# Optimization experiments

Hardware: AMD Instinct MI355X
Metric: run time of the kernel (lower is better)

The kernel has to match this reference:

```python
import jax, jax.numpy as jnp
import numpy as np

B, N, D, M, H = 16, 2048, 512, 512, 8
DH = D // H
PDE_STEPS = 3
DT = 0.01


def layer_norm(x, g, b, eps=1e-5):
    mu = x.mean(-1, keepdims=True)
    v = ((x - mu) ** 2).mean(-1, keepdims=True)
    return (x - mu) * jax.lax.rsqrt(v + eps) * g + b


def laplacian1d(f):
    # f: [B, M, D]; Neumann boundary via edge padding
    fp = jnp.pad(f, ((0, 0), (1, 1), (0, 0)), mode='edge')
    return fp[:, :-2] - 2.0 * fp[:, 1:-1] + fp[:, 2:]


def diffuse(f, coef, steps=PDE_STEPS, dt=DT):
    # explicit-Euler diffusion PDE evolution, per-channel coefficient
    for _ in range(steps):
        f = f + dt * coef * laplacian1d(f)
    return f


def setup_inputs() -> dict:
    key = jax.random.key(0)
    ks = jax.random.split(key, 10)
    s = 0.02
    return {
        'embeddings': jax.random.normal(ks[0], (B, N, D), dtype=jnp.float32),
        'positions': jax.random.uniform(ks[1], (B, N, 1), dtype=jnp.float32),
        'sigma': jnp.asarray(0.1, dtype=jnp.float32),
        'alpha': s * jax.random.normal(ks[2], (H, H), dtype=jnp.float32),
        'w_int': s * jax.random.normal(ks[3], (D, D), dtype=jnp.float32),
        'b_int': jnp.zeros((D,), dtype=jnp.float32),
        'diff_coef': 0.5 * jnp.ones((D,), dtype=jnp.float32),
        'W1': s * jax.random.normal(ks[4], (D, D), dtype=jnp.float32),
        'b1': jnp.zeros((D,), dtype=jnp.float32),
        'W2': s * jax.random.normal(ks[5], (D, D), dtype=jnp.float32),
        'b2': jnp.zeros((D,), dtype=jnp.float32),
        'evo_coef': 0.5 * jnp.ones((D,), dtype=jnp.float32),
        'ln1_g': jnp.ones((D,), dtype=jnp.float32),
        'ln1_b': jnp.zeros((D,), dtype=jnp.float32),
        'Wout': s * jax.random.normal(ks[6], (D, D), dtype=jnp.float32),
        'bout': jnp.zeros((D,), dtype=jnp.float32),
        'ln2_g': jnp.ones((D,), dtype=jnp.float32),
        'ln2_b': jnp.zeros((D,), dtype=jnp.float32),
    }


def reference(embeddings, positions, sigma, alpha, w_int, b_int, diff_coef,
              W1, b1, W2, b2, evo_coef, ln1_g, ln1_b, Wout, bout, ln2_g, ln2_b):
    # 1) RBF field projection onto uniform 1D grid in [0,1]
    grid = jnp.linspace(0.0, 1.0, M, dtype=embeddings.dtype)  # [M]
    d2 = (grid[None, :, None] - positions[..., 0][:, None, :]) ** 2  # [B,M,N]
    K = jnp.exp(-d2 / (2.0 * sigma ** 2))
    field = jnp.einsum('bmn,bnd->bmd', K, embeddings)  # [B,M,D]
    # 2) multi-head field interference: learned cross-head coupling + proj
    Fh = field.reshape(B, M, H, DH)
    mix = jnp.einsum('hk,bmkd->bmhd', alpha, Fh).reshape(B, M, D)
    field = field + mix @ w_int + b_int
    # 3) field propagation: diffusion PDE steps
    field = diffuse(field, diff_coef)
    # 4) interaction operator: pointwise gated MLP with residual
    field = field + jax.nn.gelu(field @ W1 + b1) @ W2 + b2
    # 5) field evolution: further diffusion PDE steps
    field = diffuse(field, evo_coef)
    # 6) linear field sampling back at token positions
    u = jnp.clip(positions[..., 0], 0.0, 1.0) * (M - 1)  # [B,N]
    i0 = jnp.clip(jnp.floor(u), 0, M - 2).astype(jnp.int32)
    w = (u - i0.astype(u.dtype))[..., None]  # [B,N,1]
    f0 = jnp.take_along_axis(field, i0[:, :, None], axis=1)  # [B,N,D]
    f1 = jnp.take_along_axis(field, (i0 + 1)[:, :, None], axis=1)
    sampled = (1.0 - w) * f0 + w * f1
    # 7) residual + LN, output proj (dropout=eval/identity), residual + LN
    enh = layer_norm(sampled + embeddings, ln1_g, ln1_b)
    out = enh @ Wout + bout
    out = layer_norm(out + enh, ln2_g, ln2_b)
    return out
```

## Files before the change

### kernel.cpp

```cpp
#include <hip/hip_runtime.h>
#include <hip/hip_bf16.h>
#include <math.h>

#define BB 16
#define NN 2048
#define DD 512
#define MM 512

typedef __attribute__((ext_vector_type(8))) short bf16x8;
typedef __attribute__((ext_vector_type(4))) float f32x4;

__device__ __forceinline__ short f2b(float x) {
  union { __hip_bfloat16 h; short s; } u; u.h = __float2bfloat16(x); return u.s;
}
__device__ __forceinline__ float b2f(short s) {
  union { short s2; __hip_bfloat16 h; } u; u.s2 = s; return __bfloat162float(u.h);
}
__device__ __forceinline__ float gelu_f(float x) {
  float x3 = x * x * x;
  return 0.5f * x * (1.0f + tanhf(0.79788456080286536f * (x + 0.044715f * x3)));
}

template<int BM, int BN, int NT, int WR, int WC, int ACT, int RES,
         bool BIAS, bool WB32, bool WB16, bool BATCH>
__global__ __launch_bounds__(NT) void gemm_mfma(
    const short* __restrict__ A, const short* __restrict__ BT,
    const float* __restrict__ bias, const void* __restrict__ res,
    float* __restrict__ C, short* __restrict__ Cb, int K)
{
  constexpr int WAVES = NT / 64;
  constexpr int MF = BM / WR / 16;
  constexpr int NF = BN / WC / 16;
  constexpr int WMT = BM / WR;
  constexpr int WNT = BN / WC;
  constexpr int CHA = BM / 16;
  constexpr int CHB = BN / 16;

  __shared__ short As[2][BM * 32];
  __shared__ short Bs[2][BN * 32];

  const int tid = threadIdx.x;
  const int wid = tid >> 6, lane = tid & 63;
  const int lrow = lane & 15, kg = lane >> 4;
  const int wr = (WR == 1) ? 0 : (wid >> 1);
  const int wc = (WR == 1) ? wid : (wid & 1);

  int r0, c0, z;
  if constexpr (BATCH) {
    z = blockIdx.x; r0 = blockIdx.y * BM; c0 = blockIdx.z * BN;
  } else {
    z = 0; r0 = blockIdx.x * BM; c0 = blockIdx.y * BN;
  }
  const size_t zA  = BATCH ? (size_t)z * MM * K : 0;
  const size_t zBT = BATCH ? (size_t)z * DD * K : 0;
  const size_t zC  = BATCH ? (size_t)z * MM * DD : 0;

  auto stage = [&](int bf, int kc) {
    #pragma unroll
    for (int i = 0; i < CHB / WAVES; ++i) {
      const int ch = wid * (CHB / WAVES) + i;
      const int col = ch * 16 + (lane >> 2);
      const short* gp = BT + zBT + (size_t)(c0 + col) * K + kc + (lane & 3) * 8;
      __builtin_amdgcn_global_load_lds(
          (const __attribute__((address_space(1))) void*)gp,
          (__attribute__((address_space(3))) void*)&Bs[bf][ch * 512], 16, 0, 0);
    }
    if constexpr (CHA >= WAVES) {
      #pragma unroll
      for (int i = 0; i < CHA / WAVES; ++i) {
        const int ch = wid * (CHA / WAVES) + i;
        const int row = ch * 16 + (lane >> 2);
        const short* gp = A + zA + (size_t)(r0 + row) * K + kc + (lane & 3) * 8;
        __builtin_amdgcn_global_load_lds(
            (const __attribute__((address_space(1))) void*)gp,
            (__attribute__((address_space(3))) void*)&As[bf][ch * 512], 16, 0, 0);
      }
    } else {
      if (wid < CHA) {
        const int row = wid * 16 + (lane >> 2);
        const short* gp = A + zA + (size_t)(r0 + row) * K + kc + (lane & 3) * 8;
        __builtin_amdgcn_global_load_lds(
            (const __attribute__((address_space(1))) void*)gp,
            (__attribute__((address_space(3))) void*)&As[bf][wid * 512], 16, 0, 0);
      }
    }
  };

  f32x4 acc[MF][NF];
  #pragma unroll
  for (int m = 0; m < MF; ++m)
    #pragma unroll
    for (int n = 0; n < NF; ++n) acc[m][n] = (f32x4){0.f, 0.f, 0.f, 0.f};

  stage(0, 0);
  __syncthreads();

  int buf = 0;
  for (int kc = 0; kc < K; kc += 32) {
    if (kc + 32 < K) stage(buf ^ 1, kc + 32);

    bf16x8 af[MF], bfv[NF];
    #pragma unroll
    for (int m = 0; m < MF; ++m)
      af[m] = *(const bf16x8*)&As[buf][(wr * WMT + m * 16 + lrow) * 32 + kg * 8];
    #pragma unroll
    for (int n = 0; n < NF; ++n)
      bfv[n] = *(const bf16x8*)&Bs[buf][(wc * WNT + n * 16 + lrow) * 32 + kg * 8];
    #pragma unroll
    for (int m = 0; m < MF; ++m)
      #pragma unroll
      for (int n = 0; n < NF; ++n)
        acc[m][n] = __builtin_amdgcn_mfma_f32_16x16x32_bf16(af[m], bfv[n], acc[m][n], 0, 0, 0);

    __syncthreads();
    buf ^= 1;
  }

  #pragma unroll
  for (int m = 0; m < MF; ++m) {
    #pragma unroll
    for (int n = 0; n < NF; ++n) {
      const int col = c0 + wc * WNT + n * 16 + lrow;
      const int row0 = r0 + wr * WMT + m * 16 + kg * 4;
      float bi = 0.0f;
      if constexpr (BIAS) bi = bias[col];
      #pragma unroll
      for (int r = 0; r < 4; ++r) {
        float x = acc[m][n][r] + bi;
        if constexpr (ACT == 1) x = gelu_f(x);
        const size_t off = zC + (size_t)(row0 + r) * DD + col;
        if constexpr (RES == 1) x += ((const float*)res)[off];
        if constexpr (RES == 2) x += b2f(((const short*)res)[off]);
        if constexpr (WB32) C[off] = x;
        if constexpr (WB16) Cb[off] = f2b(x);
      }
    }
  }
}

__global__ __launch_bounds__(512) void gemm_out_ln(
    const short* __restrict__ A, const short* __restrict__ BT,
    const float* __restrict__ bias, const float* __restrict__ g,
    const float* __restrict__ be, float* __restrict__ out)
{
  constexpr int BM = 64, BN = 512, K = 512;
  constexpr int WAVES = 8, CHB = BN / 16, CHA = BM / 16;

  __shared__ short As[2][BM * 32];
  __shared__ short Bs[2][BN * 32];
  __shared__ float redS[8][64], redQ[8][64];
  __shared__ float lnMu[64], lnIs[64];

  const int tid = threadIdx.x;
  const int wid = tid >> 6, lane = tid & 63;
  const int lrow = lane & 15, kg = lane >> 4;
  const int wc = wid;
  const int r0 = blockIdx.x * BM;

  auto stage = [&](int bf, int kc) {
    #pragma unroll
    for (int i = 0; i < CHB / WAVES; ++i) {
      const int ch = wid * (CHB / WAVES) + i;
      const int col = ch * 16 + (lane >> 2);
      const short* gp = BT + (size_t)col * K + kc + (lane & 3) * 8;
      __builtin_amdgcn_global_load_lds(
          (const __attribute__((address_space(1))) void*)gp,
          (__attribute__((address_space(3))) void*)&Bs[bf][ch * 512], 16, 0, 0);
    }
    if (wid < CHA) {
      const int row = wid * 16 + (lane >> 2);
      const short* gp = A + (size_t)(r0 + row) * K + kc + (lane & 3) * 8;
      __builtin_amdgcn_global_load_lds(
          (const __attribute__((address_space(1))) void*)gp,
          (__attribute__((address_space(3))) void*)&As[bf][wid * 512], 16, 0, 0);
    }
  };

  f32x4 acc[4][4];
  #pragma unroll
  for (int m = 0; m < 4; ++m)
    #pragma unroll
    for (int n = 0; n < 4; ++n) acc[m][n] = (f32x4){0.f, 0.f, 0.f, 0.f};

  stage(0, 0);
  __syncthreads();
  int buf = 0;
  for (int kc = 0; kc < K; kc += 32) {
    if (kc + 32 < K) stage(buf ^ 1, kc + 32);
    bf16x8 af[4], bfv[4];
    #pragma unroll
    for (int m = 0; m < 4; ++m)
      af[m] = *(const bf16x8*)&As[buf][(m * 16 + lrow) * 32 + kg * 8];
    #pragma unroll
    for (int n = 0; n < 4; ++n)
      bfv[n] = *(const bf16x8*)&Bs[buf][(wc * 64 + n * 16 + lrow) * 32 + kg * 8];
    #pragma unroll
    for (int m = 0; m < 4; ++m)
      #pragma unroll
      for (int n = 0; n < 4; ++n)
        acc[m][n] = __builtin_amdgcn_mfma_f32_16x16x32_bf16(af[m], bfv[n], acc[m][n], 0, 0, 0);
    __syncthreads();
    buf ^= 1;
  }

  #pragma unroll
  for (int m = 0; m < 4; ++m) {
    #pragma unroll
    for (int n = 0; n < 4; ++n) {
      const float bi = bias[wc * 64 + n * 16 + lrow];
      #pragma unroll
      for (int r = 0; r < 4; ++r) acc[m][n][r] += bi;
    }
  }
  #pragma unroll
  for (int m = 0; m < 4; ++m) {
    #pragma unroll
    for (int r = 0; r < 4; ++r) {
      float ps = acc[m][0][r] + acc[m][1][r] + acc[m][2][r] + acc[m][3][r];
      float pq = acc[m][0][r] * acc[m][0][r] + acc[m][1][r] * acc[m][1][r] +
                 acc[m][2][r] * acc[m][2][r] + acc[m][3][r] * acc[m][3][r];
      #pragma unroll
      for (int off = 8; off >= 1; off >>= 1) {
        ps += __shfl_xor(ps, off);
        pq += __shfl_xor(pq, off);
      }
      if (lrow == 0) {
        redS[wid][m * 16 + kg * 4 + r] = ps;
        redQ[wid][m * 16 + kg * 4 + r] = pq;
      }
    }
  }
  __syncthreads();
  if (tid < 64) {
    float s = 0.f, q = 0.f;
    #pragma unroll
    for (int w = 0; w < 8; ++w) { s += redS[w][tid]; q += redQ[w][tid]; }
    const float mu = s * (1.0f / 512.0f);
    const float var = q * (1.0f / 512.0f) - mu * mu;
    lnMu[tid] = mu;
    lnIs[tid] = rsqrtf(var + 1e-5f);
  }
  __syncthreads();
  #pragma unroll
  for (int m = 0; m < 4; ++m) {
    #pragma unroll
    for (int n = 0; n < 4; ++n) {
      const int col = wc * 64 + n * 16 + lrow;
      const float gc = g[col], bc = be[col];
      #pragma unroll
      for (int r = 0; r < 4; ++r) {
        const int row = m * 16 + kg * 4 + r;
        out[(size_t)(r0 + row) * DD + col] =
            (acc[m][n][r] - lnMu[row]) * lnIs[row] * gc + bc;
      }
    }
  }
}

__global__ __launch_bounds__(256) void kmat_kernel(
    const float* __restrict__ pos, const float* __restrict__ sigp,
    short* __restrict__ Kmat)
{
  const int gid = blockIdx.x * 256 + threadIdx.x;
  const int n8 = gid & 255;
  const int m  = (gid >> 8) & (MM - 1);
  const int b  = gid >> 17;
  const float s = sigp[0];
  const float inv2s2 = 1.0f / (2.0f * s * s);
  const float g = (float)m * (1.0f / 511.0f);
  const float* pp = pos + (size_t)b * NN + n8 * 8;
  const float4 p0 = *(const float4*)pp;
  const float4 p1 = *(const float4*)(pp + 4);
  const float pv[8] = {p0.x, p0.y, p0.z, p0.w, p1.x, p1.y, p1.z, p1.w};
  bf16x8 o;
  #pragma unroll
  for (int j = 0; j < 8; ++j) {
    const float d = g - pv[j];
    o[j] = f2b(__expf(-(d * d) * inv2s2));
  }
  *(bf16x8*)&Kmat[((size_t)b * MM + m) * NN + n8 * 8] = o;
}

__global__ __launch_bounds__(256) void wtrans_kernel(
    const float* __restrict__ w0, const float* __restrict__ w1,
    const float* __restrict__ w2, const float* __restrict__ w3,
    short* __restrict__ outW)
{
  __shared__ float tle[32][33];
  const int z = blockIdx.z;
  const float* W = (z == 0) ? w0 : (z == 1) ? w1 : (z == 2) ? w2 : w3;
  short* WT = outW + (size_t)z * DD * DD;
  const int bx = blockIdx.x * 32;
  const int by = blockIdx.y * 32;
  const int t = threadIdx.x;
  const int r = t >> 3, c4 = (t & 7) * 4;
  const float4 v = *(const float4*)(W + (size_t)(bx + r) * DD + by + c4);
  tle[r][c4 + 0] = v.x; tle[r][c4 + 1] = v.y; tle[r][c4 + 2] = v.z; tle[r][c4 + 3] = v.w;
  __syncthreads();
  short4 o;
  #pragma unroll
  for (int j = 0; j < 4; ++j) {
    float val = tle[c4 + j][r];
    if (z == 3 && (bx + c4 + j) == (by + r)) val += 1.0f;
    ((short*)&o)[j] = f2b(val);
  }
  *(short4*)(WT + (size_t)(by + r) * DD + bx + c4) = o;
}

__global__ __launch_bounds__(256) void embtrans_kernel(
    const float* __restrict__ emb, short* __restrict__ embT)
{
  __shared__ float tle[32][33];
  const int z = blockIdx.z;
  const int bx = blockIdx.x * 32;
  const int by = blockIdx.y * 32;
  const int t = threadIdx.x;
  const int r = t >> 3, c4 = (t & 7) * 4;
  const float4 v = *(const float4*)(emb + ((size_t)z * NN + bx + r) * DD + by + c4);
  tle[r][c4 + 0] = v.x; tle[r][c4 + 1] = v.y; tle[r][c4 + 2] = v.z; tle[r][c4 + 3] = v.w;
  __syncthreads();
  const short4 o = make_short4(f2b(tle[c4 + 0][r]), f2b(tle[c4 + 1][r]),
                               f2b(tle[c4 + 2][r]), f2b(tle[c4 + 3][r]));
  *(short4*)(embT + ((size_t)z * DD + by + r) * NN + bx + c4) = o;
}

__global__ __launch_bounds__(256) void mix_kernel(
    const float* __restrict__ field, const float* __restrict__ alpha,
    short* __restrict__ mixout)
{
  __shared__ float row[DD];
  __shared__ float al[64];
  const size_t r = blockIdx.x;
  const int t = threadIdx.x;
  const float* fr = field + r * DD;
  *(float2*)&row[t * 2] = *(const float2*)&fr[t * 2];
  if (t < 64) al[t] = alpha[t];
  __syncthreads();
  const int j = t * 2;
  const int h = j >> 6;
  const int jj = j & 63;
  float s0 = 0.0f, s1 = 0.0f;
  #pragma unroll
  for (int k = 0; k < 8; ++k) {
    const float a = al[h * 8 + k];
    const float2 v = *(const float2*)&row[k * 64 + jj];
    s0 += a * v.x;
    s1 += a * v.y;
  }
  *(short2*)&mixout[r * DD + j] = make_short2(f2b(s0), f2b(s1));
}

__device__ __forceinline__ float4 dstep(float4 fm, float4 f, float4 fp, float4 a) {
  float4 o;
  o.x = f.x + a.x * (fm.x - 2.0f * f.x + fp.x);
  o.y = f.y + a.y * (fm.y - 2.0f * f.y + fp.y);
  o.z = f.z + a.z * (fm.z - 2.0f * f.z + fp.z);
  o.w = f.w + a.w * (fm.w - 2.0f * f.w + fp.w);
  return o;
}

template<bool WB16>
__global__ __launch_bounds__(256) void diffuse3_kernel(
    const float* __restrict__ in, float* __restrict__ out,
    const float* __restrict__ coef, short* __restrict__ bfout)
{
  const size_t base = ((size_t)blockIdx.x * 256 + threadIdx.x) * 4;
  const int d = (int)(base & (DD - 1));
  const int m = (int)((base >> 9) & (MM - 1));
  const size_t rowbase = base - (size_t)m * DD;

  float4 u[7];
  #pragma unroll
  for (int o = 0; o < 7; ++o) {
    int mm = m + o - 3;
    mm = mm < 0 ? 0 : (mm > MM - 1 ? MM - 1 : mm);
    u[o] = *(const float4*)(in + rowbase + (size_t)mm * DD);
  }
  const float4 c = *(const float4*)(coef + d);
  float4 a;
  a.x = 0.01f * c.x; a.y = 0.01f * c.y; a.z = 0.01f * c.z; a.w = 0.01f * c.w;

  float4 v[5];
  #pragma unroll
  for (int o = 0; o < 5; ++o) v[o] = dstep(u[o], u[o + 1], u[o + 2], a);
  float4 w2[3];
  #pragma unroll
  for (int o = 0; o < 3; ++o) w2[o] = dstep(v[o], v[o + 1], v[o + 2], a);
  const float4 r = dstep(w2[0], w2[1], w2[2], a);

  *(float4*)(out + base) = r;
  if constexpr (WB16) {
    *(short4*)(bfout + base) = make_short4(f2b(r.x), f2b(r.y), f2b(r.z), f2b(r.w));
  }
}

__device__ __forceinline__ void ln_stats_512(float sum, float sq, float& mu, float& inv_std) {
  #pragma unroll
  for (int off = 32; off >= 1; off >>= 1) {
    sum += __shfl_down(sum, off);
    sq  += __shfl_down(sq,  off);
  }
  __shared__ float red[8];
  __shared__ float mv[2];
  const int lane = threadIdx.x & 63;
  const int wid = threadIdx.x >> 6;
  if (lane == 0) { red[wid] = sum; red[4 + wid] = sq; }
  __syncthreads();
  if (threadIdx.x == 0) {
    float ts = red[0] + red[1] + red[2] + red[3];
    float tq = red[4] + red[5] + red[6] + red[7];
    float m = ts * (1.0f / 512.0f);
    float v = tq * (1.0f / 512.0f) - m * m;
    mv[0] = m;
    mv[1] = rsqrtf(v + 1e-5f);
  }
  __syncthreads();
  mu = mv[0];
  inv_std = mv[1];
}

__global__ __launch_bounds__(256) void sample_ln_kernel(
    const float* __restrict__ field, const float* __restrict__ pos,
    const float* __restrict__ emb, const float* __restrict__ g,
    const float* __restrict__ be, short* __restrict__ enhb)
{
  const size_t row = blockIdx.x;
  const int b = (int)(row >> 11);
  const int t = threadIdx.x;

  const float p = pos[row];
  const float u = fminf(fmaxf(p, 0.0f), 1.0f) * 511.0f;
  int i0 = (int)floorf(u);
  if (i0 > MM - 2) i0 = MM - 2;
  if (i0 < 0) i0 = 0;
  const float w = u - (float)i0;

  const float* f0 = field + ((size_t)b * MM + i0) * DD;
  const int j = t * 2;
  const float2 a0 = *(const float2*)(f0 + j);
  const float2 a1 = *(const float2*)(f0 + DD + j);
  const float2 e = *(const float2*)(emb + row * DD + j);
  const float sx = (1.0f - w) * a0.x + w * a1.x + e.x;
  const float sy = (1.0f - w) * a0.y + w * a1.y + e.y;

  float mu, is;
  ln_stats_512(sx + sy, sx * sx + sy * sy, mu, is);

  const float2 gg = *(const float2*)(g + j);
  const float2 bb2 = *(const float2*)(be + j);
  *(short2*)&enhb[row * DD + j] = make_short2(
      f2b((sx - mu) * is * gg.x + bb2.x),
      f2b((sy - mu) * is * gg.y + bb2.y));
}


extern "C" void kernel_launch(void* const* d_in, const int* in_sizes, int n_in,
                              void* d_out, int out_size, void* d_ws, size_t ws_size,
                              hipStream_t stream)
{
  const float* emb   = (const float*)d_in[0];
  const float* pos   = (const float*)d_in[1];
  const float* sigma = (const float*)d_in[2];
  const float* alpha = (const float*)d_in[3];
  const float* w_int = (const float*)d_in[4];
  const float* b_int = (const float*)d_in[5];
  const float* diffc = (const float*)d_in[6];
  const float* W1    = (const float*)d_in[7];
  const float* b1    = (const float*)d_in[8];
  const float* W2    = (const float*)d_in[9];
  const float* b2    = (const float*)d_in[10];
  const float* evoc  = (const float*)d_in[11];
  const float* ln1g  = (const float*)d_in[12];
  const float* ln1b  = (const float*)d_in[13];
  const float* Wout  = (const float*)d_in[14];
  const float* bout  = (const float*)d_in[15];
  const float* ln2g  = (const float*)d_in[16];
  const float* ln2b  = (const float*)d_in[17];

  float* out = (float*)d_out;
  char* w = (char*)d_ws;
  float* f0    = (float*)w;
  short* Kmat  = (short*)(w + 16777216);
  float* f1    = (float*)(w + 16777216);
  short* mixb  = (short*)(w + 33554432);
  short* hb    = (short*)(w + 41943040);
  short* embT  = (short*)(w + 50331648);
  short* enhb  = (short*)(w + 50331648);
  short* wT    = (short*)(w + 83886080);
  short* wintT = wT;
  short* w1T   = wT + (size_t)DD * DD;
  short* w2T   = wT + (size_t)2 * DD * DD;
  short* woutT = wT + (size_t)3 * DD * DD;

  const dim3 blk(256);
  const int diff_blocks = BB * MM * DD / 4 / 256;

  wtrans_kernel<<<dim3(16, 16, 4), blk, 0, stream>>>(w_int, W1, W2, Wout, wT);
  embtrans_kernel<<<dim3(64, 16, 16), blk, 0, stream>>>(emb, embT);
  kmat_kernel<<<dim3(BB * MM * NN / 8 / 256), blk, 0, stream>>>(pos, sigma, Kmat);

  gemm_mfma<64, 128, 256, 1, 4, 0, 0, false, true, false, true>
      <<<dim3(BB, MM / 64, DD / 128), blk, 0, stream>>>(
          Kmat, embT, nullptr, nullptr, f0, nullptr, NN);

  mix_kernel<<<dim3(BB * MM), blk, 0, stream>>>(f0, alpha, mixb);
  gemm_mfma<64, 128, 256, 1, 4, 0, 1, true, true, false, false>
      <<<dim3(BB * MM / 64, DD / 128), blk, 0, stream>>>(
          mixb, wintT, b_int, f0, f0, nullptr, DD);

  diffuse3_kernel<true><<<dim3(diff_blocks), blk, 0, stream>>>(f0, f1, diffc, mixb);

  gemm_mfma<64, 128, 256, 1, 4, 1, 0, true, false, true, false>
      <<<dim3(BB * MM / 64, DD / 128), blk, 0, stream>>>(
          mixb, w1T, b1, nullptr, nullptr, hb, DD);
  gemm_mfma<64, 128, 256, 1, 4, 0, 1, true, true, false, false>
      <<<dim3(BB * MM / 64, DD / 128), blk, 0, stream>>>(
          hb, w2T, b2, f1, f1, nullptr, DD);

  diffuse3_kernel<false><<<dim3(diff_blocks), blk, 0, stream>>>(f1, f0, evoc, nullptr);

  sample_ln_kernel<<<dim3(BB * NN), blk, 0, stream>>>(f0, pos, emb, ln1g, ln1b, enhb);

  gemm_out_ln<<<dim3(BB * NN / 64), dim3(512), 0, stream>>>(
      enhb, woutT, bout, ln2g, ln2b, out);
}
```

Measured before the change: 347.9 us.

## Fold head-mixing and residual into effective weight; enlarge output GEMM tile

Replaces the separate mix kernel and the residual add with a precomputed effective weight Weff = I + alpha-mixed w_int. The interference step then becomes a single GEMM on the bf16 field written directly by the RBF projection GEMM. This removes one elementwise pass and the fp32 field round trip. The residual path now goes through bf16 instead of fp32, which costs some precision. Separately, the output GEMM+LN kernel moves to 128-row tiles with 1024 threads (16 waves), so each staged copy of the weight tile is reused by more rows.

```diff
diff --git a/kernel.cpp b/kernel.cpp
--- a/kernel.cpp
+++ b/kernel.cpp
@@ -138,23 +138,25 @@
   }
 }
 
-__global__ __launch_bounds__(512) void gemm_out_ln(
+__global__ __launch_bounds__(1024) void gemm_out_ln(
     const short* __restrict__ A, const short* __restrict__ BT,
     const float* __restrict__ bias, const float* __restrict__ g,
     const float* __restrict__ be, float* __restrict__ out)
 {
-  constexpr int BM = 64, BN = 512, K = 512;
-  constexpr int WAVES = 8, CHB = BN / 16, CHA = BM / 16;
+  constexpr int BM = 128, BN = 512, K = 512;
+  constexpr int WAVES = 16, CHB = BN / 16, CHA = BM / 16;
 
   __shared__ short As[2][BM * 32];
   __shared__ short Bs[2][BN * 32];
-  __shared__ float redS[8][64], redQ[8][64];
-  __shared__ float lnMu[64], lnIs[64];
+  __shared__ float redS[8][BM];
+  __shared__ float redQ[8][BM];
+  __shared__ float lnMu[BM], lnIs[BM];
 
   const int tid = threadIdx.x;
   const int wid = tid >> 6, lane = tid & 63;
   const int lrow = lane & 15, kg = lane >> 4;
-  const int wc = wid;
+  const int wr = wid >> 3;
+  const int wc = wid & 7;
   const int r0 = blockIdx.x * BM;
 
   auto stage = [&](int bf, int kc) {
@@ -190,7 +192,7 @@
     bf16x8 af[4], bfv[4];
     #pragma unroll
     for (int m = 0; m < 4; ++m)
-      af[m] = *(const bf16x8*)&As[buf][(m * 16 + lrow) * 32 + kg * 8];
+      af[m] = *(const bf16x8*)&As[buf][(wr * 64 + m * 16 + lrow) * 32 + kg * 8];
     #pragma unroll
     for (int n = 0; n < 4; ++n)
       bfv[n] = *(const bf16x8*)&Bs[buf][(wc * 64 + n * 16 + lrow) * 32 + kg * 8];
@@ -225,13 +227,14 @@
         pq += __shfl_xor(pq, off);
       }
       if (lrow == 0) {
-        redS[wid][m * 16 + kg * 4 + r] = ps;
-        redQ[wid][m * 16 + kg * 4 + r] = pq;
+        const int row = wr * 64 + m * 16 + kg * 4 + r;
+        redS[wc][row] = ps;
+        redQ[wc][row] = pq;
       }
     }
   }
   __syncthreads();
-  if (tid < 64) {
+  if (tid < BM) {
     float s = 0.f, q = 0.f;
     #pragma unroll
     for (int w = 0; w < 8; ++w) { s += redS[w][tid]; q += redQ[w][tid]; }
@@ -249,12 +252,84 @@
       const float gc = g[col], bc = be[col];
       #pragma unroll
       for (int r = 0; r < 4; ++r) {
-        const int row = m * 16 + kg * 4 + r;
+        const int row = wr * 64 + m * 16 + kg * 4 + r;
         out[(size_t)(r0 + row) * DD + col] =
             (acc[m][n][r] - lnMu[row]) * lnIs[row] * gc + bc;
       }
     }
   }
+}
+
+__global__ __launch_bounds__(256) void weff_kernel(
+    const float* __restrict__ alpha, const float* __restrict__ w_int,
+    short* __restrict__ WeffT)
+{
+  __shared__ float tle[32][33];
+  const int q0 = blockIdx.x * 32;
+  const int c0 = blockIdx.y * 32;
+  const int t = threadIdx.x;
+  const int r = t >> 3, c4 = (t & 7) * 4;
+  const int kq = q0 >> 6;
+  const int jb = q0 & 63;
+
+  float v[4] = {0.f, 0.f, 0.f, 0.f};
+  #pragma unroll
+  for (int h = 0; h < 8; ++h) {
+    const float a = alpha[h * 8 + kq];
+    const float4 wv = *(const float4*)(w_int + (size_t)(h * 64 + jb + r) * DD + c0 + c4);
+    v[0] += a * wv.x; v[1] += a * wv.y; v[2] += a * wv.z; v[3] += a * wv.w;
+  }
+  #pragma unroll
+  for (int j = 0; j < 4; ++j) {
+    if (q0 + r == c0 + c4 + j) v[j] += 1.0f;
+    tle[r][c4 + j] = v[j];
+  }
+  __syncthreads();
+  const short4 o = make_short4(f2b(tle[c4 + 0][r]), f2b(tle[c4 + 1][r]),
+                               f2b(tle[c4 + 2][r]), f2b(tle[c4 + 3][r]));
+  *(short4*)(WeffT + (size_t)(c0 + r) * DD + q0 + c4) = o;
+}
+
+__global__ __launch_bounds__(256) void wtrans_kernel(
+    const float* __restrict__ w1, const float* __restrict__ w2,
+    const float* __restrict__ w3, short* __restrict__ outW)
+{
+  __shared__ float tle[32][33];
+  const int z = blockIdx.z;
+  const float* W = (z == 0) ? w1 : (z == 1) ? w2 : w3;
+  short* WT = outW + (size_t)(z + 1) * DD * DD;
+  const int bx = blockIdx.x * 32;
+  const int by = blockIdx.y * 32;
+  const int t = threadIdx.x;
+  const int r = t >> 3, c4 = (t & 7) * 4;
+  const float4 v = *(const float4*)(W + (size_t)(bx + r) * DD + by + c4);
+  tle[r][c4 + 0] = v.x; tle[r][c4 + 1] = v.y; tle[r][c4 + 2] = v.z; tle[r][c4 + 3] = v.w;
+  __syncthreads();
+  short4 o;
+  #pragma unroll
+  for (int j = 0; j < 4; ++j) {
+    float val = tle[c4 + j][r];
+    if (z == 2 && (bx + c4 + j) == (by + r)) val += 1.0f;
+    ((short*)&o)[j] = f2b(val);
+  }
+  *(short4*)(WT + (size_t)(by + r) * DD + bx + c4) = o;
+}
+
+__global__ __launch_bounds__(256) void embtrans_kernel(
+    const float* __restrict__ emb, short* __restrict__ embT)
+{
+  __shared__ float tle[32][33];
+  const int z = blockIdx.z;
+  const int bx = blockIdx.x * 32;
+  const int by = blockIdx.y * 32;
+  const int t = threadIdx.x;
+  const int r = t >> 3, c4 = (t & 7) * 4;
+  const float4 v = *(const float4*)(emb + ((size_t)z * NN + bx + r) * DD + by + c4);
+  tle[r][c4 + 0] = v.x; tle[r][c4 + 1] = v.y; tle[r][c4 + 2] = v.z; tle[r][c4 + 3] = v.w;
+  __syncthreads();
+  const short4 o = make_short4(f2b(tle[c4 + 0][r]), f2b(tle[c4 + 1][r]),
+                               f2b(tle[c4 + 2][r]), f2b(tle[c4 + 3][r]));
+  *(short4*)(embT + ((size_t)z * DD + by + r) * NN + bx + c4) = o;
 }
 
 __global__ __launch_bounds__(256) void kmat_kernel(
@@ -279,75 +354,6 @@
     o[j] = f2b(__expf(-(d * d) * inv2s2));
   }
   *(bf16x8*)&Kmat[((size_t)b * MM + m) * NN + n8 * 8] = o;
-}
-
-__global__ __launch_bounds__(256) void wtrans_kernel(
-    const float* __restrict__ w0, const float* __restrict__ w1,
-    const float* __restrict__ w2, const float* __restrict__ w3,
-    short* __restrict__ outW)
-{
-  __shared__ float tle[32][33];
-  const int z = blockIdx.z;
-  const float* W = (z == 0) ? w0 : (z == 1) ? w1 : (z == 2) ? w2 : w3;
-  short* WT = outW + (size_t)z * DD * DD;
-  const int bx = blockIdx.x * 32;
-  const int by = blockIdx.y * 32;
-  const int t = threadIdx.x;
-  const int r = t >> 3, c4 = (t & 7) * 4;
-  const float4 v = *(const float4*)(W + (size_t)(bx + r) * DD + by + c4);
-  tle[r][c4 + 0] = v.x; tle[r][c4 + 1] = v.y; tle[r][c4 + 2] = v.z; tle[r][c4 + 3] = v.w;
-  __syncthreads();
-  short4 o;
-  #pragma unroll
-  for (int j = 0; j < 4; ++j) {
-    float val = tle[c4 + j][r];
-    if (z == 3 && (bx + c4 + j) == (by + r)) val += 1.0f;
-    ((short*)&o)[j] = f2b(val);
-  }
-  *(short4*)(WT + (size_t)(by + r) * DD + bx + c4) = o;
-}
-
-__global__ __launch_bounds__(256) void embtrans_kernel(
-    const float* __restrict__ emb, short* __restrict__ embT)
-{
-  __shared__ float tle[32][33];
-  const int z = blockIdx.z;
-  const int bx = blockIdx.x * 32;
-  const int by = blockIdx.y * 32;
-  const int t = threadIdx.x;
-  const int r = t >> 3, c4 = (t & 7) * 4;
-  const float4 v = *(const float4*)(emb + ((size_t)z * NN + bx + r) * DD + by + c4);
-  tle[r][c4 + 0] = v.x; tle[r][c4 + 1] = v.y; tle[r][c4 + 2] = v.z; tle[r][c4 + 3] = v.w;
-  __syncthreads();
-  const short4 o = make_short4(f2b(tle[c4 + 0][r]), f2b(tle[c4 + 1][r]),
-                               f2b(tle[c4 + 2][r]), f2b(tle[c4 + 3][r]));
-  *(short4*)(embT + ((size_t)z * DD + by + r) * NN + bx + c4) = o;
-}
-
-__global__ __launch_bounds__(256) void mix_kernel(
-    const float* __restrict__ field, const float* __restrict__ alpha,
-    short* __restrict__ mixout)
-{
-  __shared__ float row[DD];
-  __shared__ float al[64];
-  const size_t r = blockIdx.x;
-  const int t = threadIdx.x;
-  const float* fr = field + r * DD;
-  *(float2*)&row[t * 2] = *(const float2*)&fr[t * 2];
-  if (t < 64) al[t] = alpha[t];
-  __syncthreads();
-  const int j = t * 2;
-  const int h = j >> 6;
-  const int jj = j & 63;
-  float s0 = 0.0f, s1 = 0.0f;
-  #pragma unroll
-  for (int k = 0; k < 8; ++k) {
-    const float a = al[h * 8 + k];
-    const float2 v = *(const float2*)&row[k * 64 + jj];
-    s0 += a * v.x;
-    s1 += a * v.y;
-  }
-  *(short2*)&mixout[r * DD + j] = make_short2(f2b(s0), f2b(s1));
 }
 
 __device__ __forceinline__ float4 dstep(float4 fm, float4 f, float4 fp, float4 a) {
@@ -479,40 +485,41 @@
 
   float* out = (float*)d_out;
   char* w = (char*)d_ws;
-  float* f0    = (float*)w;
-  short* Kmat  = (short*)(w + 16777216);
-  float* f1    = (float*)(w + 16777216);
-  short* mixb  = (short*)(w + 33554432);
-  short* hb    = (short*)(w + 41943040);
-  short* embT  = (short*)(w + 50331648);
-  short* enhb  = (short*)(w + 50331648);
-  short* wT    = (short*)(w + 83886080);
-  short* wintT = wT;
-  short* w1T   = wT + (size_t)DD * DD;
-  short* w2T   = wT + (size_t)2 * DD * DD;
-  short* woutT = wT + (size_t)3 * DD * DD;
+  float* f0      = (float*)w;
+  short* Kmat    = (short*)(w + 16777216);
+  float* f1      = (float*)(w + 16777216);
+  short* hb      = (short*)(w + 33554432);
+  short* fieldb2 = (short*)(w + 41943040);
+  short* embT    = (short*)(w + 50331648);
+  short* enhb    = (short*)(w + 50331648);
+  short* wT      = (short*)(w + 83886080);
+  short* weffT   = wT;
+  short* w1T     = wT + (size_t)DD * DD;
+  short* w2T     = wT + (size_t)2 * DD * DD;
+  short* woutT   = wT + (size_t)3 * DD * DD;
+  short* fieldb  = (short*)(w + 85983232);
 
   const dim3 blk(256);
   const int diff_blocks = BB * MM * DD / 4 / 256;
 
-  wtrans_kernel<<<dim3(16, 16, 4), blk, 0, stream>>>(w_int, W1, W2, Wout, wT);
+  weff_kernel<<<dim3(16, 16), blk, 0, stream>>>(alpha, w_int, weffT);
+  wtrans_kernel<<<dim3(16, 16, 3), blk, 0, stream>>>(W1, W2, Wout, wT);
   embtrans_kernel<<<dim3(64, 16, 16), blk, 0, stream>>>(emb, embT);
   kmat_kernel<<<dim3(BB * MM * NN / 8 / 256), blk, 0, stream>>>(pos, sigma, Kmat);
 
-  gemm_mfma<64, 128, 256, 1, 4, 0, 0, false, true, false, true>
+  gemm_mfma<64, 128, 256, 1, 4, 0, 0, false, false, true, true>
       <<<dim3(BB, MM / 64, DD / 128), blk, 0, stream>>>(
-          Kmat, embT, nullptr, nullptr, f0, nullptr, NN);
-
-  mix_kernel<<<dim3(BB * MM), blk, 0, stream>>>(f0, alpha, mixb);
-  gemm_mfma<64, 128, 256, 1, 4, 0, 1, true, true, false, false>
+          Kmat, embT, nullptr, nullptr, nullptr, fieldb, NN);
+
+  gemm_mfma<64, 128, 256, 1, 4, 0, 0, true, true, false, false>
       <<<dim3(BB * MM / 64, DD / 128), blk, 0, stream>>>(
-          mixb, wintT, b_int, f0, f0, nullptr, DD);
-
-  diffuse3_kernel<true><<<dim3(diff_blocks), blk, 0, stream>>>(f0, f1, diffc, mixb);
+          fieldb, weffT, b_int, nullptr, f0, nullptr, DD);
+
+  diffuse3_kernel<true><<<dim3(diff_blocks), blk, 0, stream>>>(f0, f1, diffc, fieldb2);
 
   gemm_mfma<64, 128, 256, 1, 4, 1, 0, true, false, true, false>
       <<<dim3(BB * MM / 64, DD / 128), blk, 0, stream>>>(
-          mixb, w1T, b1, nullptr, nullptr, hb, DD);
+          fieldb2, w1T, b1, nullptr, nullptr, hb, DD);
   gemm_mfma<64, 128, 256, 1, 4, 0, 1, true, true, false, false>
       <<<dim3(BB * MM / 64, DD / 128), blk, 0, stream>>>(
           hb, w2T, b2, f1, f1, nullptr, DD);
@@ -521,6 +528,6 @@
 
   sample_ln_kernel<<<dim3(BB * NN), blk, 0, stream>>>(f0, pos, emb, ln1g, ln1b, enhb);
 
-  gemm_out_ln<<<dim3(BB * NN / 64), dim3(512), 0, stream>>>(
+  gemm_out_ln<<<dim3(BB * NN / 128), dim3(1024), 0, stream>>>(
       enhb, woutT, bout, ln2g, ln2b, out);
 }
```

Result: faster. 334.7 us (-3.8%).
